# Kernel tuning notes

Measured on AMD Instinct MI355X. Metric: run time of the kernel, lower is better.

Reference implementation:

```python
import jax, jax.numpy as jnp
import numpy as np

NUM_CODES = 8192
DIM = 256
TAU = 1.0
KL_WEIGHT = 0.01
COMMIT_WEIGHT = 0.25
B, C, P = 8, 64, 32


def setup_inputs() -> dict:
    key = jax.random.key(0)
    kz, kc = jax.random.split(key)
    z = jax.random.normal(kz, (B, C, P, DIM), dtype=jnp.float32)
    # nn.init.normal_(codebook.weight, std=1/sqrt(dim))
    codebook = jax.random.normal(kc, (NUM_CODES, DIM), dtype=jnp.float32) / jnp.sqrt(jnp.float32(DIM))
    return {"z": z, "codebook": codebook}


def reference(z, codebook):
    Bq, Cq, Pq, D = z.shape
    flat = z.reshape(-1, D)                                  # (N, D)
    logits = flat @ codebook.T                               # (N, num_codes)
    # training path: gumbel-softmax (hard=False), fixed key for determinism
    g = jax.random.gumbel(jax.random.key(42), logits.shape, dtype=logits.dtype)
    soft_one_hot = jax.nn.softmax((logits + g) / TAU, axis=-1)
    z_q = (soft_one_hot @ codebook).reshape(Bq, Cq, Pq, D)
    # KL to uniform prior: sum(qy * log(qy * K + 1e-10))
    log_qy = jax.nn.log_softmax(logits, axis=-1)
    qy = jnp.exp(log_qy)
    kl_loss = KL_WEIGHT * jnp.mean(jnp.sum(qy * jnp.log(qy * NUM_CODES + 1e-10), axis=-1))
    codes = jnp.argmax(logits, axis=-1).reshape(Bq, Cq, Pq)
    commit_loss = COMMIT_WEIGHT * jnp.mean((jax.lax.stop_gradient(z_q) - z) ** 2)
    z_q_st = z + jax.lax.stop_gradient(z_q - z)              # straight-through
    total_loss = commit_loss + kl_loss
    return (z_q_st, total_loss, codes)
```

## Files before the change

### kernel.cpp

```cpp
#include <hip/hip_runtime.h>
#include <stdint.h>
#include <math.h>

#define N_ROWS   16384
#define N_CODES  8192
#define DIMV     256
#define RT       32
#define CK       32
#define NCHUNK   (N_CODES / CK)
#define OUT_ZQ_N ((size_t)N_ROWS * DIMV)
#define OUT_LOSS OUT_ZQ_N
#define OUT_CODE (OUT_ZQ_N + 1)

#define WS_CBHI 0u
#define WS_CBLO 4194304u
#define WS_CBT  8388608u
#define WS_ACC  12582912u
#define WS_NEED (12582912u + 64u)

#define CB1H_OFF  0
#define CB1L_OFF  16896
#define CBT_OFF   33792
#define P_OFF     50688
#define P_SPLIT   2560
#define P_ROW     80
#define S2B_OFF   55808
#define SKL_OFF   56064
#define TKL_OFF   56320
#define V1B_OFF   56576
#define I1B_OFF   56832
#define V2B_OFF   57088
#define I2B_OFF   57344
#define SMEM_BYTES 57600
#define ZT_ROWF   260

typedef __attribute__((ext_vector_type(8))) short short8;
typedef __attribute__((ext_vector_type(4))) float float4v;

typedef __attribute__((address_space(1))) uint32_t g_u32;
typedef __attribute__((address_space(3))) uint32_t l_u32;

__device__ __forceinline__ void dma16(const void* gsrc, void* ldst) {
  __builtin_amdgcn_global_load_lds((g_u32*)gsrc, (l_u32*)ldst, 16, 0, 0);
}

__device__ __forceinline__ uint32_t rotl32(uint32_t x, int r) {
  return (x << r) | (x >> (32 - r));
}

__device__ __forceinline__ uint32_t threefry_bits(uint32_t c) {
  const uint32_t k0 = 0u, k1 = 42u;
  const uint32_t k2 = 0x1BD11BDAu ^ k0 ^ k1;
  uint32_t x0 = 0u + k0;
  uint32_t x1 = c + k1;
#define TF_R(r) { x0 += x1; x1 = rotl32(x1, r); x1 ^= x0; }
  TF_R(13) TF_R(15) TF_R(26) TF_R(6)
  x0 += k1; x1 += k2 + 1u;
  TF_R(17) TF_R(29) TF_R(16) TF_R(24)
  x0 += k2; x1 += k0 + 2u;
  TF_R(13) TF_R(15) TF_R(26) TF_R(6)
  x0 += k0; x1 += k1 + 3u;
  TF_R(17) TF_R(29) TF_R(16) TF_R(24)
  x0 += k1; x1 += k2 + 4u;
  TF_R(13) TF_R(15) TF_R(26) TF_R(6)
  x0 += k2; x1 += k0 + 5u;
#undef TF_R
  return x0 ^ x1;
}

__device__ __forceinline__ float gumbel_at_v1(uint32_t idx) {
  uint32_t bits = threefry_bits(idx);
  float u = __uint_as_float((bits >> 9) | 0x3f800000u) - 1.0f;
  u = fmaxf(u, 1.17549435e-38f);
  return -logf(-logf(u));
}

__device__ __forceinline__ unsigned short f2bf(float x) {
  uint32_t u = __float_as_uint(x);
  u += 0x7fffu + ((u >> 16) & 1u);
  return (unsigned short)(u >> 16);
}
__device__ __forceinline__ float bf2f(unsigned short h) {
  return __uint_as_float(((uint32_t)h) << 16);
}

__global__ __launch_bounds__(256)
void vq_prep(const float* __restrict__ cb, char* __restrict__ ws) {
  __shared__ unsigned short lhs[32 * 260];
  const int c = blockIdx.x;
  const int tid = threadIdx.x;
  const int k0 = c * 32;
  unsigned short* cbhi = (unsigned short*)(ws + WS_CBHI);
  unsigned short* cblo = (unsigned short*)(ws + WS_CBLO);
  unsigned short* cbt  = (unsigned short*)(ws + WS_CBT);
#pragma unroll
  for (int i = 0; i < 8; ++i) {
    int F = tid + i * 256;
    int code = F >> 6, d4 = (F & 63) * 4;
    float4 v = *(const float4*)(cb + (size_t)(k0 + code) * DIMV + d4);
    unsigned short h0 = f2bf(v.x), h1 = f2bf(v.y), h2 = f2bf(v.z), h3 = f2bf(v.w);
    unsigned short l0 = f2bf(v.x - bf2f(h0)), l1 = f2bf(v.y - bf2f(h1));
    unsigned short l2 = f2bf(v.z - bf2f(h2)), l3 = f2bf(v.w - bf2f(h3));
    ushort4 hv = {h0, h1, h2, h3};
    ushort4 lv = {l0, l1, l2, l3};
    *(ushort4*)(cbhi + (size_t)(k0 + code) * DIMV + d4) = hv;
    *(ushort4*)(cblo + (size_t)(k0 + code) * DIMV + d4) = lv;
    *(ushort4*)(&lhs[code * 260 + d4]) = hv;
  }
  __syncthreads();
  const int d = tid;
  unsigned short vals[32];
#pragma unroll
  for (int cc = 0; cc < 32; ++cc) vals[cc] = lhs[cc * 260 + d];
  unsigned short* base = cbt + (size_t)c * 8192 + (size_t)d * 32;
#pragma unroll
  for (int j = 0; j < 8; ++j) {
    ushort4 w = {vals[4 * j], vals[4 * j + 1], vals[4 * j + 2], vals[4 * j + 3]};
    *(ushort4*)(base + j * 4) = w;
  }
}

__global__ __launch_bounds__(256, 2)
void vq_main_v2(const float* __restrict__ z, const float* __restrict__ cb,
                float* __restrict__ out, char* __restrict__ ws) {
  __shared__ __align__(16) char sm[SMEM_BYTES];
  const int tid  = threadIdx.x;
  const int wave = tid >> 6;
  const int lane = tid & 63;
  const int quad = lane >> 4;
  const int n    = lane & 15;
  const int mt   = wave & 1;
  const int nt   = wave >> 1;
  const int r0   = blockIdx.x * RT;
  const int myrow = mt * 16 + quad * 4;
  const char* cbhi_b = ws + WS_CBHI;
  const char* cblo_b = ws + WS_CBLO;
  const char* cbt_b  = ws + WS_CBT;
  float* wsA = (float*)(ws + WS_ACC);

  {
    float* zts = (float*)sm;
#pragma unroll
    for (int i = 0; i < 8; ++i) {
      int F = tid + i * 256;
      int row = F >> 6, d4 = (F & 63) * 4;
      *(float4*)(zts + row * ZT_ROWF + d4) =
          *(const float4*)(z + (size_t)(r0 + row) * DIMV + d4);
    }
  }
  __syncthreads();
  short8 zhi[8], zlo[8];
  {
    const float* zts = (const float*)sm;
    const int rowl = mt * 16 + n;
#pragma unroll
    for (int ks = 0; ks < 8; ++ks) {
      const float* zp = zts + rowl * ZT_ROWF + ks * 32 + quad * 8;
      float4 f0 = *(const float4*)zp;
      float4 f1 = *(const float4*)(zp + 4);
      float ff0[4] = {f0.x, f0.y, f0.z, f0.w};
      float ff1[4] = {f1.x, f1.y, f1.z, f1.w};
#pragma unroll
      for (int j = 0; j < 4; ++j) {
        unsigned short h = f2bf(ff0[j]);
        zhi[ks][j] = (short)h;
        zlo[ks][j] = (short)f2bf(ff0[j] - bf2f(h));
      }
#pragma unroll
      for (int j = 0; j < 4; ++j) {
        unsigned short h = f2bf(ff1[j]);
        zhi[ks][4 + j] = (short)h;
        zlo[ks][4 + j] = (short)f2bf(ff1[j] - bf2f(h));
      }
    }
  }

  float skl[4] = {0.f, 0.f, 0.f, 0.f};
  float tkl[4] = {0.f, 0.f, 0.f, 0.f};
  float s2l[4] = {0.f, 0.f, 0.f, 0.f};
  float v1[4], v2[4];
  int   i1[4], i2[4];
  uint32_t idxr[4];
#pragma unroll
  for (int r = 0; r < 4; ++r) {
    v1[r] = -INFINITY; v2[r] = -INFINITY;
    i1[r] = 0x7fffffff; i2[r] = 0x7fffffff;
    idxr[r] = (uint32_t)(r0 + myrow + r) * (uint32_t)N_CODES + (uint32_t)(nt * 16 + n);
  }
  float4v acc2[8];
#pragma unroll
  for (int t = 0; t < 8; ++t) acc2[t] = (float4v){0.f, 0.f, 0.f, 0.f};

  for (int c = 0; c < NCHUNK; ++c) {
    const int k0 = c * CK;
    __syncthreads();
#pragma unroll
    for (int i = 0; i < 4; ++i) {
      int b = wave * 4 + i;
      dma16(cbhi_b + (size_t)(k0 + 2 * b) * 512 + (size_t)lane * 16,
            sm + CB1H_OFF + b * 1056);
      dma16(cblo_b + (size_t)(k0 + 2 * b) * 512 + (size_t)lane * 16,
            sm + CB1L_OFF + b * 1056);
      dma16(cbt_b + (size_t)c * 16384 + (size_t)b * 1024 + (size_t)lane * 16,
            sm + CBT_OFF + b * 1056);
    }
    __syncthreads();

    float4v acc1 = (float4v){0.f, 0.f, 0.f, 0.f};
    {
      const int kc = nt * 16 + n;
      const char* bbase = sm + CB1H_OFF + (kc >> 1) * 1056 + (kc & 1) * 512 + quad * 16;
#pragma unroll
      for (int ks = 0; ks < 8; ++ks) {
        short8 bh = *(const short8*)(bbase + ks * 64);
        short8 bl = *(const short8*)(bbase + (CB1L_OFF - CB1H_OFF) + ks * 64);
        acc1 = __builtin_amdgcn_mfma_f32_16x16x32_bf16(zhi[ks], bh, acc1, 0, 0, 0);
        acc1 = __builtin_amdgcn_mfma_f32_16x16x32_bf16(zhi[ks], bl, acc1, 0, 0, 0);
        acc1 = __builtin_amdgcn_mfma_f32_16x16x32_bf16(zlo[ks], bh, acc1, 0, 0, 0);
      }
    }

    const int codeg0 = k0 + nt * 16 + n;
#pragma unroll
    for (int r = 0; r < 4; ++r) {
      float l = acc1[r];
      uint32_t bits = threefry_bits(idxr[r]);
      idxr[r] += 32u;
      float u = __uint_as_float((bits >> 9) | 0x3f800000u) - 1.0f;
      float h = u - 1.0f;
      float uu = fmaxf(u, 1.17549435e-38f);
      float t_hw = -0.69314718056f * __log2f(uu);
      float poly = 1.0f + h * (-0.5f + h * (0.33333333f + h * (-0.25f)));
      float t = (h > -0.015625f) ? (-h * poly) : t_hw;
      float e = __expf(l);
      skl[r] += e;
      tkl[r] = fmaf(e, l, tkl[r]);
      bool b1 = l > v1[r];
      bool b2 = l > v2[r];
      v2[r] = b1 ? v1[r] : (b2 ? l : v2[r]);
      i2[r] = b1 ? i1[r] : (b2 ? codeg0 : i2[r]);
      v1[r] = b1 ? l : v1[r];
      i1[r] = b1 ? codeg0 : i1[r];
      float p = e * __builtin_amdgcn_rcpf(t) * 6.1442123533282097e-06f;
      unsigned short ph = f2bf(p);
      float pfl = bf2f(ph);
      unsigned short plo = f2bf(p - pfl);
      s2l[r] += pfl + bf2f(plo);
      int prow = myrow + r;
      int pcol = nt * 16 + n;
      *(unsigned short*)(sm + P_OFF + prow * P_ROW + pcol * 2) = ph;
      *(unsigned short*)(sm + P_OFF + P_SPLIT + prow * P_ROW + pcol * 2) = plo;
    }
    __syncthreads();

    {
      short8 pah0 = *(const short8*)(sm + P_OFF + n * P_ROW + quad * 16);
      short8 pal0 = *(const short8*)(sm + P_OFF + P_SPLIT + n * P_ROW + quad * 16);
      short8 pah1 = *(const short8*)(sm + P_OFF + (16 + n) * P_ROW + quad * 16);
      short8 pal1 = *(const short8*)(sm + P_OFF + P_SPLIT + (16 + n) * P_ROW + quad * 16);
#pragma unroll
      for (int t = 0; t < 4; ++t) {
        int dt = wave * 4 + t;
        short8 bb = *(const short8*)(sm + CBT_OFF + dt * 1056 + n * 64 + quad * 16);
        acc2[t * 2 + 0] = __builtin_amdgcn_mfma_f32_16x16x32_bf16(pah0, bb, acc2[t * 2 + 0], 0, 0, 0);
        acc2[t * 2 + 0] = __builtin_amdgcn_mfma_f32_16x16x32_bf16(pal0, bb, acc2[t * 2 + 0], 0, 0, 0);
        acc2[t * 2 + 1] = __builtin_amdgcn_mfma_f32_16x16x32_bf16(pah1, bb, acc2[t * 2 + 1], 0, 0, 0);
        acc2[t * 2 + 1] = __builtin_amdgcn_mfma_f32_16x16x32_bf16(pal1, bb, acc2[t * 2 + 1], 0, 0, 0);
      }
    }
  }

#pragma unroll
  for (int m = 1; m <= 8; m <<= 1) {
#pragma unroll
    for (int r = 0; r < 4; ++r) {
      s2l[r] += __shfl_xor(s2l[r], m);
      skl[r] += __shfl_xor(skl[r], m);
      tkl[r] += __shfl_xor(tkl[r], m);
      float ov1 = __shfl_xor(v1[r], m); int oi1 = __shfl_xor(i1[r], m);
      float ov2 = __shfl_xor(v2[r], m); int oi2 = __shfl_xor(i2[r], m);
      bool bb = (ov1 > v1[r]) || (ov1 == v1[r] && oi1 < i1[r]);
      float w1 = bb ? ov1 : v1[r]; int wi1 = bb ? oi1 : i1[r];
      float lv = bb ? v1[r] : ov1; int li = bb ? i1[r] : oi1;
      float cv = bb ? ov2 : v2[r]; int ci = bb ? oi2 : i2[r];
      bool b2 = (lv > cv) || (lv == cv && li < ci);
      v1[r] = w1; i1[r] = wi1;
      v2[r] = b2 ? lv : cv; i2[r] = b2 ? li : ci;
    }
  }
  if (n == 0) {
    int off = (nt * 32 + myrow) * 4;
    float4 fs = {s2l[0], s2l[1], s2l[2], s2l[3]};
    *(float4*)(sm + S2B_OFF + off) = fs;
    float4 fk = {skl[0], skl[1], skl[2], skl[3]};
    *(float4*)(sm + SKL_OFF + off) = fk;
    float4 ft = {tkl[0], tkl[1], tkl[2], tkl[3]};
    *(float4*)(sm + TKL_OFF + off) = ft;
    float4 f1 = {v1[0], v1[1], v1[2], v1[3]};
    *(float4*)(sm + V1B_OFF + off) = f1;
    int4 g1 = {i1[0], i1[1], i1[2], i1[3]};
    *(int4*)(sm + I1B_OFF + off) = g1;
    float4 f2 = {v2[0], v2[1], v2[2], v2[3]};
    *(float4*)(sm + V2B_OFF + off) = f2;
    int4 g2 = {i2[0], i2[1], i2[2], i2[3]};
    *(int4*)(sm + I2B_OFF + off) = g2;
  }
  {
    float* zts = (float*)sm;
#pragma unroll
    for (int i = 0; i < 8; ++i) {
      int F = tid + i * 256;
      int row = F >> 6, d4 = (F & 63) * 4;
      *(float4*)(zts + row * ZT_ROWF + d4) =
          *(const float4*)(z + (size_t)(r0 + row) * DIMV + d4);
    }
  }
  __syncthreads();

  const float* zts = (const float*)sm;
  if (tid < 32) {
    int r = tid;
    const float* sklb = (const float*)(sm + SKL_OFF);
    const float* tklb = (const float*)(sm + TKL_OFF);
    float S = sklb[r] + sklb[32 + r];
    float T = tklb[r] + tklb[32 + r];
    float klr = T / S - __logf(S) + 9.010913347279288f;
#pragma unroll
    for (int m = 1; m <= 16; m <<= 1) klr += __shfl_xor(klr, m);
    if (r == 0) atomicAdd(&wsA[0], klr);
    int cidx[4];
    cidx[0] = *(const int*)(sm + I1B_OFF + r * 4);
    cidx[1] = *(const int*)(sm + I2B_OFF + r * 4);
    cidx[2] = *(const int*)(sm + I1B_OFF + 128 + r * 4);
    cidx[3] = *(const int*)(sm + I2B_OFF + 128 + r * 4);
    const float* zp = zts + r * ZT_ROWF;
    double best = -1.0e300;
    int bi = 0x7fffffff;
#pragma unroll
    for (int cnd = 0; cnd < 4; ++cnd) {
      const float* cp = cb + (size_t)cidx[cnd] * DIMV;
      double d = 0.0;
      for (int dd = 0; dd < DIMV; dd += 4) {
        float4 zv = *(const float4*)(zp + dd);
        float4 xv = *(const float4*)(cp + dd);
        d += (double)zv.x * xv.x + (double)zv.y * xv.y +
             (double)zv.z * xv.z + (double)zv.w * xv.w;
      }
      if (d > best || (d == best && cidx[cnd] < bi)) { best = d; bi = cidx[cnd]; }
    }
    out[OUT_CODE + (size_t)(r0 + r)] = (float)bi;
  }

  float invm0[4], invm1[4];
  {
    const float* s2b = (const float*)(sm + S2B_OFF);
#pragma unroll
    for (int e = 0; e < 4; ++e) {
      float Sa = s2b[quad * 4 + e] + s2b[32 + quad * 4 + e];
      float Sb = s2b[16 + quad * 4 + e] + s2b[32 + 16 + quad * 4 + e];
      invm0[e] = 1.0f / Sa;
      invm1[e] = 1.0f / Sb;
    }
  }
  float cpart = 0.f;
#pragma unroll
  for (int t = 0; t < 4; ++t) {
    int dim = (wave * 4 + t) * 16 + n;
#pragma unroll
    for (int ms = 0; ms < 2; ++ms) {
      float4v a = acc2[t * 2 + ms];
#pragma unroll
      for (int e = 0; e < 4; ++e) {
        int row = ms * 16 + quad * 4 + e;
        float q = a[e] * (ms ? invm1[e] : invm0[e]);
        float zv = zts[row * ZT_ROWF + dim];
        float err = q - zv;
        cpart += err * err;
        out[(size_t)(r0 + row) * DIMV + dim] = zv + err;
      }
    }
  }
#pragma unroll
  for (int m = 1; m <= 32; m <<= 1) cpart += __shfl_xor(cpart, m);
  if (lane == 0) atomicAdd(&wsA[1], cpart);
}

#define ZSTRIDE  260
#define CSTRIDE  260
#define PSTRIDE  36
#define RSTRIDE  17

__global__ __launch_bounds__(256, 2)
void vq_main_v1(const float* __restrict__ z, const float* __restrict__ cb,
                float* __restrict__ out, float* __restrict__ ws_acc) {
  __shared__ float zt[RT * ZSTRIDE];
  __shared__ float cbt[CK * CSTRIDE];
  __shared__ float ptile[RT * PSTRIDE];
  __shared__ float redb[RT * RSTRIDE];
  __shared__ float m2s[RT], s2s[RT], scls[RT];

  const int tid = threadIdx.x;
  const int r0  = blockIdx.x * RT;
#pragma unroll
  for (int p = 0; p < 8; ++p) {
    int q = tid + p * 256;
    int i = q >> 6, c4 = (q & 63) * 4;
    *(float4*)(&zt[i * ZSTRIDE + c4]) = *(const float4*)(z + (size_t)(r0 + i) * DIMV + c4);
  }
  if (tid < RT) { m2s[tid] = -INFINITY; s2s[tid] = 0.f; scls[tid] = 0.f; }
  const int tr = tid & 15, tk = tid >> 4, rowg = tid >> 6;
  const int d4 = (tid & 63) * 4;
  float c_m[2][2], c_s[2][2], c_t[2][2];
  int   c_i[2][2];
#pragma unroll
  for (int a = 0; a < 2; ++a)
#pragma unroll
    for (int b = 0; b < 2; ++b) { c_m[a][b] = -INFINITY; c_s[a][b] = 0.f; c_t[a][b] = 0.f; c_i[a][b] = 0; }
  float acc2[8][4];
#pragma unroll
  for (int j = 0; j < 8; ++j)
#pragma unroll
    for (int e = 0; e < 4; ++e) acc2[j][e] = 0.f;
  __syncthreads();
  for (int c = 0; c < NCHUNK; ++c) {
    const int k0 = c * CK;
#pragma unroll
    for (int p = 0; p < 8; ++p) {
      int q = tid + p * 256;
      int i = q >> 6, c4 = (q & 63) * 4;
      *(float4*)(&cbt[i * CSTRIDE + c4]) = *(const float4*)(cb + (size_t)(k0 + i) * DIMV + c4);
    }
    __syncthreads();
    float l00 = 0.f, l01 = 0.f, l10 = 0.f, l11 = 0.f;
    {
      const float* zp0 = &zt[tr * ZSTRIDE];
      const float* zp1 = &zt[(tr + 16) * ZSTRIDE];
      const float* bp0 = &cbt[tk * CSTRIDE];
      const float* bp1 = &cbt[(tk + 16) * CSTRIDE];
#pragma unroll 4
      for (int d = 0; d < DIMV; d += 4) {
        float4 a0 = *(const float4*)(zp0 + d);
        float4 a1 = *(const float4*)(zp1 + d);
        float4 b0 = *(const float4*)(bp0 + d);
        float4 b1 = *(const float4*)(bp1 + d);
        l00 += a0.x*b0.x + a0.y*b0.y + a0.z*b0.z + a0.w*b0.w;
        l01 += a0.x*b1.x + a0.y*b1.y + a0.z*b1.z + a0.w*b1.w;
        l10 += a1.x*b0.x + a1.y*b0.y + a1.z*b0.z + a1.w*b0.w;
        l11 += a1.x*b1.x + a1.y*b1.y + a1.z*b1.z + a1.w*b1.w;
      }
    }
    float lv2[2][2] = {{l00, l01}, {l10, l11}};
    float a2[2][2];
#pragma unroll
    for (int a = 0; a < 2; ++a) {
      int grow = r0 + tr + a * 16;
#pragma unroll
      for (int b = 0; b < 2; ++b) {
        int gk = k0 + tk + b * 16;
        float g  = gumbel_at_v1((uint32_t)grow * (uint32_t)N_CODES + (uint32_t)gk);
        float lv = lv2[a][b];
        a2[a][b] = lv + g;
        if (lv > c_m[a][b]) {
          float sc = expf(c_m[a][b] - lv);
          c_s[a][b] = c_s[a][b] * sc + 1.0f;
          c_t[a][b] = c_t[a][b] * sc + lv;
          c_m[a][b] = lv;
          c_i[a][b] = gk;
        } else {
          float e = expf(lv - c_m[a][b]);
          c_s[a][b] += e;
          c_t[a][b] += e * lv;
        }
      }
    }
    redb[tr * RSTRIDE + tk]        = fmaxf(a2[0][0], a2[0][1]);
    redb[(tr + 16) * RSTRIDE + tk] = fmaxf(a2[1][0], a2[1][1]);
    __syncthreads();
    if (tid < RT) {
      float cm = -INFINITY;
#pragma unroll
      for (int j = 0; j < 16; ++j) cm = fmaxf(cm, redb[tid * RSTRIDE + j]);
      float m2n = fmaxf(m2s[tid], cm);
      scls[tid] = expf(m2s[tid] - m2n);
      m2s[tid]  = m2n;
    }
    __syncthreads();
#pragma unroll
    for (int a = 0; a < 2; ++a) {
      int row = tr + a * 16;
      float m2r = m2s[row];
      float p0 = expf(a2[a][0] - m2r);
      float p1 = expf(a2[a][1] - m2r);
      ptile[row * PSTRIDE + tk]      = p0;
      ptile[row * PSTRIDE + tk + 16] = p1;
      redb[row * RSTRIDE + tk] = p0 + p1;
    }
    __syncthreads();
    if (tid < RT) {
      float ss = 0.f;
#pragma unroll
      for (int j = 0; j < 16; ++j) ss += redb[tid * RSTRIDE + j];
      s2s[tid] = s2s[tid] * scls[tid] + ss;
    }
#pragma unroll
    for (int j = 0; j < 8; ++j) {
      float sc = scls[rowg * 8 + j];
      acc2[j][0] *= sc; acc2[j][1] *= sc; acc2[j][2] *= sc; acc2[j][3] *= sc;
    }
    for (int k4 = 0; k4 < CK; k4 += 4) {
      float4 cb0 = *(const float4*)(&cbt[(k4 + 0) * CSTRIDE + d4]);
      float4 cb1v = *(const float4*)(&cbt[(k4 + 1) * CSTRIDE + d4]);
      float4 cb2 = *(const float4*)(&cbt[(k4 + 2) * CSTRIDE + d4]);
      float4 cb3 = *(const float4*)(&cbt[(k4 + 3) * CSTRIDE + d4]);
#pragma unroll
      for (int j = 0; j < 8; ++j) {
        float4 p4 = *(const float4*)(&ptile[(rowg * 8 + j) * PSTRIDE + k4]);
        acc2[j][0] += p4.x*cb0.x + p4.y*cb1v.x + p4.z*cb2.x + p4.w*cb3.x;
        acc2[j][1] += p4.x*cb0.y + p4.y*cb1v.y + p4.z*cb2.y + p4.w*cb3.y;
        acc2[j][2] += p4.x*cb0.z + p4.y*cb1v.z + p4.z*cb2.z + p4.w*cb3.z;
        acc2[j][3] += p4.x*cb0.w + p4.y*cb1v.w + p4.z*cb2.w + p4.w*cb3.w;
      }
    }
    __syncthreads();
  }
  float* kbuf = cbt;
#pragma unroll
  for (int a = 0; a < 2; ++a) {
    float m0 = c_m[a][0], m1v = c_m[a][1];
    float m, s, t; int bi;
    if (m0 >= m1v) {
      float e = expf(m1v - m0);
      m = m0; s = c_s[a][0] + c_s[a][1] * e; t = c_t[a][0] + c_t[a][1] * e;
    } else {
      float e = expf(m0 - m1v);
      m = m1v; s = c_s[a][0] * e + c_s[a][1]; t = c_t[a][0] * e + c_t[a][1];
    }
    if (m0 > m1v)      bi = c_i[a][0];
    else if (m1v > m0) bi = c_i[a][1];
    else               bi = min(c_i[a][0], c_i[a][1]);
    int row = tr + a * 16;
    kbuf[row * 65 + tk * 4 + 0] = m;
    kbuf[row * 65 + tk * 4 + 1] = s;
    kbuf[row * 65 + tk * 4 + 2] = t;
    kbuf[row * 65 + tk * 4 + 3] = (float)bi;
  }
  __syncthreads();
  if (tid < RT) {
    int r = tid;
    float M = -INFINITY, S = 0.f, T = 0.f, BM = -INFINITY;
    int BI = 0x7fffffff;
    for (int j = 0; j < 16; ++j) {
      float m  = kbuf[r * 65 + j * 4 + 0];
      float s  = kbuf[r * 65 + j * 4 + 1];
      float t  = kbuf[r * 65 + j * 4 + 2];
      int   bi = (int)kbuf[r * 65 + j * 4 + 3];
      if (m <= M) {
        float e = expf(m - M);
        S += s * e; T += t * e;
      } else {
        float e = expf(M - m);
        S = S * e + s; T = T * e + t; M = m;
      }
      if (m > BM || (m == BM && bi < BI)) { BM = m; BI = bi; }
    }
    float kl = logf((float)N_CODES) + T / S - M - logf(S);
    atomicAdd(&ws_acc[0], kl);
    out[OUT_CODE + (size_t)(r0 + r)] = (float)BI;
  }
  float cpart = 0.f;
#pragma unroll
  for (int j = 0; j < 8; ++j) {
    int row  = rowg * 8 + j;
    int grow = r0 + row;
    float inv = 1.0f / s2s[row];
    float4 zv = *(const float4*)(&zt[row * ZSTRIDE + d4]);
    float q0 = acc2[j][0] * inv, q1 = acc2[j][1] * inv;
    float q2 = acc2[j][2] * inv, q3 = acc2[j][3] * inv;
    float e0 = q0 - zv.x, e1 = q1 - zv.y, e2 = q2 - zv.z, e3 = q3 - zv.w;
    cpart += e0*e0 + e1*e1 + e2*e2 + e3*e3;
    float4 o;
    o.x = zv.x + e0; o.y = zv.y + e1; o.z = zv.z + e2; o.w = zv.w + e3;
    *(float4*)(&out[(size_t)grow * DIMV + d4]) = o;
  }
#pragma unroll
  for (int off = 32; off > 0; off >>= 1) cpart += __shfl_down(cpart, off, 64);
  __syncthreads();
  if ((tid & 63) == 0) redb[tid >> 6] = cpart;
  __syncthreads();
  if (tid == 0) {
    float cs = redb[0] + redb[1] + redb[2] + redb[3];
    atomicAdd(&ws_acc[1], cs);
  }
}

__global__ void vq_finalize(const float* __restrict__ ws_acc, float* __restrict__ out) {
  if (threadIdx.x == 0 && blockIdx.x == 0) {
    float kl = 0.01f * (ws_acc[0] / (float)N_ROWS);
    float cm = 0.25f * (ws_acc[1] / (float)OUT_ZQ_N);
    out[OUT_LOSS] = cm + kl;
  }
}

extern "C" void kernel_launch(void* const* d_in, const int* in_sizes, int n_in,
                              void* d_out, int out_size, void* d_ws, size_t ws_size,
                              hipStream_t stream) {
  (void)in_sizes; (void)n_in; (void)out_size;
  const float* z  = (const float*)d_in[0];
  const float* cb = (const float*)d_in[1];
  float* out = (float*)d_out;
  if (ws_size >= (size_t)WS_NEED) {
    char* ws = (char*)d_ws;
    hipMemsetAsync(ws + WS_ACC, 0, 8, stream);
    vq_prep<<<256, 256, 0, stream>>>(cb, ws);
    vq_main_v2<<<N_ROWS / RT, 256, 0, stream>>>(z, cb, out, ws);
    vq_finalize<<<1, 64, 0, stream>>>((const float*)(ws + WS_ACC), out);
  } else {
    float* ws = (float*)d_ws;
    hipMemsetAsync(ws, 0, 8, stream);
    vq_main_v1<<<N_ROWS / RT, 256, 0, stream>>>(z, cb, out, ws);
    vq_finalize<<<1, 64, 0, stream>>>(ws, out);
  }
}
```

Baseline: 793.5 us.

## Software-pipeline chunk loop: overlap codebook DMA and softmax with MFMA across chunks

Restructures the main chunk loop into a one-stage software pipeline. The MFMA logits for chunk c are computed while the gumbel/softmax epilogue runs on chunk c-1's logits, and the DMA for the next codebook chunk is issued before the second GEMM. The transposed codebook tile is double-buffered and the LDS padding is changed. It also splits the three-term split-bf16 accumulation into independent accumulators to shorten the MFMA dependency chain, and uses a rotate builtin in threefry. The cost is more LDS (occupancy risk) and more live registers.

```diff
diff --git a/kernel.cpp b/kernel.cpp
--- a/kernel.cpp
+++ b/kernel.cpp
@@ -19,19 +19,21 @@
 #define WS_NEED (12582912u + 64u)
 
 #define CB1H_OFF  0
-#define CB1L_OFF  16896
-#define CBT_OFF   33792
-#define P_OFF     50688
+#define CB1L_OFF  16640
+#define CB1_BS    1040
+#define CBT0_OFF  33280
+#define CBT1_OFF  49664
+#define P_OFF     66048
 #define P_SPLIT   2560
 #define P_ROW     80
-#define S2B_OFF   55808
-#define SKL_OFF   56064
-#define TKL_OFF   56320
-#define V1B_OFF   56576
-#define I1B_OFF   56832
-#define V2B_OFF   57088
-#define I2B_OFF   57344
-#define SMEM_BYTES 57600
+#define S2B_OFF   71168
+#define SKL_OFF   71424
+#define TKL_OFF   71680
+#define V1B_OFF   71936
+#define I1B_OFF   72192
+#define V2B_OFF   72448
+#define I2B_OFF   72704
+#define SMEM_BYTES 72960
 #define ZT_ROWF   260
 
 typedef __attribute__((ext_vector_type(8))) short short8;
@@ -45,7 +47,7 @@
 }
 
 __device__ __forceinline__ uint32_t rotl32(uint32_t x, int r) {
-  return (x << r) | (x >> (32 - r));
+  return __builtin_rotateleft32(x, (uint32_t)r);
 }
 
 __device__ __forceinline__ uint32_t threefry_bits(uint32_t c) {
@@ -174,6 +176,16 @@
       }
     }
   }
+  __syncthreads();
+
+#pragma unroll
+  for (int i = 0; i < 4; ++i) {
+    int b = wave * 4 + i;
+    dma16(cbhi_b + (size_t)(2 * b) * 512 + (size_t)lane * 16, sm + CB1H_OFF + b * CB1_BS);
+    dma16(cblo_b + (size_t)(2 * b) * 512 + (size_t)lane * 16, sm + CB1L_OFF + b * CB1_BS);
+    dma16(cbt_b + (size_t)b * 1024 + (size_t)lane * 16, sm + CBT0_OFF + b * 1024);
+  }
+  __syncthreads();
 
   float skl[4] = {0.f, 0.f, 0.f, 0.f};
   float tkl[4] = {0.f, 0.f, 0.f, 0.f};
@@ -190,70 +202,71 @@
   float4v acc2[8];
 #pragma unroll
   for (int t = 0; t < 8; ++t) acc2[t] = (float4v){0.f, 0.f, 0.f, 0.f};
-
-  for (int c = 0; c < NCHUNK; ++c) {
-    const int k0 = c * CK;
-    __syncthreads();
-#pragma unroll
-    for (int i = 0; i < 4; ++i) {
-      int b = wave * 4 + i;
-      dma16(cbhi_b + (size_t)(k0 + 2 * b) * 512 + (size_t)lane * 16,
-            sm + CB1H_OFF + b * 1056);
-      dma16(cblo_b + (size_t)(k0 + 2 * b) * 512 + (size_t)lane * 16,
-            sm + CB1L_OFF + b * 1056);
-      dma16(cbt_b + (size_t)c * 16384 + (size_t)b * 1024 + (size_t)lane * 16,
-            sm + CBT_OFF + b * 1056);
-    }
-    __syncthreads();
-
-    float4v acc1 = (float4v){0.f, 0.f, 0.f, 0.f};
-    {
-      const int kc = nt * 16 + n;
-      const char* bbase = sm + CB1H_OFF + (kc >> 1) * 1056 + (kc & 1) * 512 + quad * 16;
+  float4v accP = (float4v){0.f, 0.f, 0.f, 0.f};
+
+  const int kc = nt * 16 + n;
+  const char* bbase = sm + CB1H_OFF + (kc >> 1) * CB1_BS + (kc & 1) * 512 + quad * 16;
+
+  for (int c = 0; c <= NCHUNK; ++c) {
+    float4v hh = (float4v){0.f, 0.f, 0.f, 0.f};
+    float4v hl = (float4v){0.f, 0.f, 0.f, 0.f};
+    float4v lh = (float4v){0.f, 0.f, 0.f, 0.f};
+    if (c < NCHUNK) {
 #pragma unroll
       for (int ks = 0; ks < 8; ++ks) {
         short8 bh = *(const short8*)(bbase + ks * 64);
         short8 bl = *(const short8*)(bbase + (CB1L_OFF - CB1H_OFF) + ks * 64);
-        acc1 = __builtin_amdgcn_mfma_f32_16x16x32_bf16(zhi[ks], bh, acc1, 0, 0, 0);
-        acc1 = __builtin_amdgcn_mfma_f32_16x16x32_bf16(zhi[ks], bl, acc1, 0, 0, 0);
-        acc1 = __builtin_amdgcn_mfma_f32_16x16x32_bf16(zlo[ks], bh, acc1, 0, 0, 0);
-      }
-    }
-
-    const int codeg0 = k0 + nt * 16 + n;
-#pragma unroll
-    for (int r = 0; r < 4; ++r) {
-      float l = acc1[r];
-      uint32_t bits = threefry_bits(idxr[r]);
-      idxr[r] += 32u;
-      float u = __uint_as_float((bits >> 9) | 0x3f800000u) - 1.0f;
-      float h = u - 1.0f;
-      float uu = fmaxf(u, 1.17549435e-38f);
-      float t_hw = -0.69314718056f * __log2f(uu);
-      float poly = 1.0f + h * (-0.5f + h * (0.33333333f + h * (-0.25f)));
-      float t = (h > -0.015625f) ? (-h * poly) : t_hw;
-      float e = __expf(l);
-      skl[r] += e;
-      tkl[r] = fmaf(e, l, tkl[r]);
-      bool b1 = l > v1[r];
-      bool b2 = l > v2[r];
-      v2[r] = b1 ? v1[r] : (b2 ? l : v2[r]);
-      i2[r] = b1 ? i1[r] : (b2 ? codeg0 : i2[r]);
-      v1[r] = b1 ? l : v1[r];
-      i1[r] = b1 ? codeg0 : i1[r];
-      float p = e * __builtin_amdgcn_rcpf(t) * 6.1442123533282097e-06f;
-      unsigned short ph = f2bf(p);
-      float pfl = bf2f(ph);
-      unsigned short plo = f2bf(p - pfl);
-      s2l[r] += pfl + bf2f(plo);
-      int prow = myrow + r;
-      int pcol = nt * 16 + n;
-      *(unsigned short*)(sm + P_OFF + prow * P_ROW + pcol * 2) = ph;
-      *(unsigned short*)(sm + P_OFF + P_SPLIT + prow * P_ROW + pcol * 2) = plo;
-    }
+        hh = __builtin_amdgcn_mfma_f32_16x16x32_bf16(zhi[ks], bh, hh, 0, 0, 0);
+        hl = __builtin_amdgcn_mfma_f32_16x16x32_bf16(zhi[ks], bl, hl, 0, 0, 0);
+        lh = __builtin_amdgcn_mfma_f32_16x16x32_bf16(zlo[ks], bh, lh, 0, 0, 0);
+      }
+    }
+    if (c > 0) {
+      const int codeg0 = (c - 1) * CK + nt * 16 + n;
+#pragma unroll
+      for (int r = 0; r < 4; ++r) {
+        float l = accP[r];
+        uint32_t bits = threefry_bits(idxr[r]);
+        idxr[r] += 32u;
+        float u = __uint_as_float((bits >> 9) | 0x3f800000u) - 1.0f;
+        float h = u - 1.0f;
+        float uu = fmaxf(u, 1.17549435e-38f);
+        float t_hw = -0.69314718056f * __log2f(uu);
+        float poly = 1.0f + h * (-0.5f + h * (0.33333333f + h * (-0.25f)));
+        float t = (h > -0.015625f) ? (-h * poly) : t_hw;
+        float e = __expf(l);
+        skl[r] += e;
+        tkl[r] = fmaf(e, l, tkl[r]);
+        bool b1 = l > v1[r];
+        bool b2 = l > v2[r];
+        v2[r] = b1 ? v1[r] : (b2 ? l : v2[r]);
+        i2[r] = b1 ? i1[r] : (b2 ? codeg0 : i2[r]);
+        v1[r] = b1 ? l : v1[r];
+        i1[r] = b1 ? codeg0 : i1[r];
+        float p = e * __builtin_amdgcn_rcpf(t) * 6.1442123533282097e-06f;
+        unsigned short ph = f2bf(p);
+        float pfl = bf2f(ph);
+        unsigned short plo = f2bf(p - pfl);
+        s2l[r] += pfl + bf2f(plo);
+        int prow = myrow + r;
+        *(unsigned short*)(sm + P_OFF + prow * P_ROW + kc * 2) = ph;
+        *(unsigned short*)(sm + P_OFF + P_SPLIT + prow * P_ROW + kc * 2) = plo;
+      }
+    }
+    accP = hh + hl + lh;
+
     __syncthreads();
-
-    {
+    if (c + 1 < NCHUNK) {
+      const size_t k1 = (size_t)(c + 1) * CK;
+#pragma unroll
+      for (int i = 0; i < 4; ++i) {
+        int b = wave * 4 + i;
+        dma16(cbhi_b + (k1 + 2 * b) * 512 + (size_t)lane * 16, sm + CB1H_OFF + b * CB1_BS);
+        dma16(cblo_b + (k1 + 2 * b) * 512 + (size_t)lane * 16, sm + CB1L_OFF + b * CB1_BS);
+      }
+    }
+    if (c > 0) {
+      const char* cbtb = sm + ((c & 1) ? CBT0_OFF : CBT1_OFF);
       short8 pah0 = *(const short8*)(sm + P_OFF + n * P_ROW + quad * 16);
       short8 pal0 = *(const short8*)(sm + P_OFF + P_SPLIT + n * P_ROW + quad * 16);
       short8 pah1 = *(const short8*)(sm + P_OFF + (16 + n) * P_ROW + quad * 16);
@@ -261,11 +274,20 @@
 #pragma unroll
       for (int t = 0; t < 4; ++t) {
         int dt = wave * 4 + t;
-        short8 bb = *(const short8*)(sm + CBT_OFF + dt * 1056 + n * 64 + quad * 16);
+        short8 bb = *(const short8*)(cbtb + dt * 1024 + n * 64 + quad * 16);
         acc2[t * 2 + 0] = __builtin_amdgcn_mfma_f32_16x16x32_bf16(pah0, bb, acc2[t * 2 + 0], 0, 0, 0);
         acc2[t * 2 + 0] = __builtin_amdgcn_mfma_f32_16x16x32_bf16(pal0, bb, acc2[t * 2 + 0], 0, 0, 0);
         acc2[t * 2 + 1] = __builtin_amdgcn_mfma_f32_16x16x32_bf16(pah1, bb, acc2[t * 2 + 1], 0, 0, 0);
         acc2[t * 2 + 1] = __builtin_amdgcn_mfma_f32_16x16x32_bf16(pal1, bb, acc2[t * 2 + 1], 0, 0, 0);
+      }
+    }
+    __syncthreads();
+    if (c + 1 < NCHUNK) {
+#pragma unroll
+      for (int i = 0; i < 4; ++i) {
+        int b = wave * 4 + i;
+        dma16(cbt_b + (size_t)(c + 1) * 16384 + (size_t)b * 1024 + (size_t)lane * 16,
+              sm + ((c & 1) ? CBT0_OFF : CBT1_OFF) + b * 1024);
       }
     }
   }
```

Result: slower. 901.0 us (+13.5%).
